# Kernel optimization log

Hardware: AMD Instinct MI355X
Metric: run time of the kernel (lower is better)

The kernel has to match this reference:

```python
import jax, jax.numpy as jnp
import numpy as np

GRAVITY, MAIN_THRUST, SIDE_TORQUE, DT = 10.0, 6.0, 1.0, 0.02
H_OBS = jnp.array([[1, 0, 0, 0, 0, 0],
                   [0, 1, 0, 0, 0, 0],
                   [0, 0, 0, 0, 1, 0]], dtype=jnp.float32)  # (3,6)


def build_psd(log_diag, off_diag, dim):
    rows, cols = np.tril_indices(dim, -1)  # row-major, same order as torch.tril_indices
    L = jnp.zeros((dim, dim), dtype=log_diag.dtype)
    L = L.at[jnp.arange(dim), jnp.arange(dim)].set(jnp.exp(log_diag))
    L = L.at[rows, cols].set(off_diag)
    return L @ L.T + 1e-6 * jnp.eye(dim, dtype=log_diag.dtype)


def setup_inputs() -> dict:
    key = jax.random.key(0)
    B = 524288
    ks = jax.random.split(key, 8)
    z = jax.random.normal(ks[0], (B, 3), dtype=jnp.float32)
    u = jax.random.uniform(ks[1], (B, 2), dtype=jnp.float32)
    x_prev = jax.random.normal(ks[2], (B, 6), dtype=jnp.float32)
    A = 0.1 * jax.random.normal(ks[3], (B, 6, 6), dtype=jnp.float32)
    P_prev = jnp.einsum('bij,bkj->bik', A, A) + 0.5 * jnp.eye(6, dtype=jnp.float32)
    q_log_diag = jnp.array([-3.0, -3.0, -2.0, -2.0, -3.0, -2.0], dtype=jnp.float32)
    q_off_diag = 0.01 * jax.random.normal(ks[4], (15,), dtype=jnp.float32)
    r_log_diag = jnp.array([-2.0, -2.0, -2.0], dtype=jnp.float32)
    r_off_diag = 0.01 * jax.random.normal(ks[5], (3,), dtype=jnp.float32)
    return {"z": z, "u": u, "x_prev": x_prev, "P_prev": P_prev,
            "q_log_diag": q_log_diag, "q_off_diag": q_off_diag,
            "r_log_diag": r_log_diag, "r_off_diag": r_off_diag}


def _dynamics(x, u):
    px, py, vx, vy, theta, omega = (x[:, i] for i in range(6))
    main_power = jnp.clip(u[:, 0], 0.0, 1.0)
    lateral = u[:, 1]
    sin_th, cos_th = jnp.sin(theta), jnp.cos(theta)
    ax = -MAIN_THRUST * sin_th * main_power
    ay = MAIN_THRUST * cos_th * main_power - GRAVITY
    alpha = SIDE_TORQUE * lateral
    new_vx = vx + ax * DT
    new_vy = vy + ay * DT
    new_omega = omega + alpha * DT
    new_px = px + new_vx * DT
    new_py = py + new_vy * DT
    new_theta = theta + new_omega * DT
    return jnp.stack([new_px, new_py, new_vx, new_vy, new_theta, new_omega], axis=-1)


def _dynamics_jacobian(x, u):
    B = x.shape[0]
    theta = x[:, 4]
    main_power = jnp.clip(u[:, 0], 0.0, 1.0)
    sin_th, cos_th = jnp.sin(theta), jnp.cos(theta)
    Tm = MAIN_THRUST * main_power
    d = jnp.arange(6)
    F = jnp.zeros((B, 6, 6), dtype=x.dtype).at[:, d, d].set(1.0)
    F = F.at[:, 0, 2].set(DT).at[:, 1, 3].set(DT).at[:, 4, 5].set(DT)
    F = F.at[:, 2, 4].set(-Tm * cos_th * DT)
    F = F.at[:, 3, 4].set(-Tm * sin_th * DT)
    F = F.at[:, 0, 4].set(-Tm * cos_th * (DT * DT))
    F = F.at[:, 1, 4].set(-Tm * sin_th * (DT * DT))
    return F


def reference(z, u, x_prev, P_prev, q_log_diag, q_off_diag, r_log_diag, r_off_diag):
    Q = build_psd(q_log_diag, q_off_diag, 6)
    R = build_psd(r_log_diag, r_off_diag, 3)
    H = H_OBS
    # predict
    x_pred = _dynamics(x_prev, u)                              # (B,6)
    F = _dynamics_jacobian(x_prev, u)                          # (B,6,6)
    P_pred = jnp.einsum('bij,bjk,blk->bil', F, P_prev, F) + Q  # F P F^T + Q
    # update
    z_pred = jnp.einsum('ij,bj->bi', H, x_pred)                # (B,3)
    y = z - z_pred
    HP = jnp.einsum('ij,bjk->bik', H, P_pred)                  # (B,3,6)
    S = jnp.einsum('bij,kj->bik', HP, H) + R                   # (B,3,3)
    K = jnp.swapaxes(jnp.linalg.solve(S, HP), -1, -2)          # (B,6,3)
    x_upd = x_pred + jnp.einsum('bij,bj->bi', K, y)
    IKH = jnp.eye(6, dtype=x_pred.dtype) - jnp.einsum('bij,jk->bik', K, H)
    P_upd = (jnp.einsum('bij,bjk,blk->bil', IKH, P_pred, IKH)
             + jnp.einsum('bij,jk,blk->bil', K, R, K))          # Joseph form
    return (x_upd, P_upd)
```

## Files before the change

### kernel.cpp

```cpp
#include <hip/hip_runtime.h>

namespace {
constexpr float GRAVITY     = 10.0f;
constexpr float MAIN_THRUST = 6.0f;
constexpr float DT          = 0.02f;
constexpr int   BLK         = 256;
constexpr int   CHUNK       = 256;
constexpr int   ROWPAD      = 44;
}

typedef float nfloat4 __attribute__((ext_vector_type(4)));
typedef float nfloat2 __attribute__((ext_vector_type(2)));

__global__ void qr_precompute(const float* __restrict__ qld,
                              const float* __restrict__ qod,
                              const float* __restrict__ rld,
                              const float* __restrict__ rod,
                              float* __restrict__ out)
{
    if (threadIdx.x != 0 || blockIdx.x != 0) return;
    float L[6][6];
    for (int i = 0; i < 6; ++i)
        for (int j = 0; j < 6; ++j) L[i][j] = 0.0f;
    for (int i = 0; i < 6; ++i) L[i][i] = expf(qld[i]);
    L[1][0] = qod[0];
    L[2][0] = qod[1];  L[2][1] = qod[2];
    L[3][0] = qod[3];  L[3][1] = qod[4];  L[3][2] = qod[5];
    L[4][0] = qod[6];  L[4][1] = qod[7];  L[4][2] = qod[8];  L[4][3] = qod[9];
    L[5][0] = qod[10]; L[5][1] = qod[11]; L[5][2] = qod[12]; L[5][3] = qod[13];
    L[5][4] = qod[14];
    for (int i = 0; i < 6; ++i)
        for (int j = 0; j < 6; ++j) {
            float s = 0.0f;
            const int m = i < j ? i : j;
            for (int k = 0; k <= m; ++k) s += L[i][k] * L[j][k];
            if (i == j) s += 1e-6f;
            out[i * 6 + j] = s;
        }
    const float rd0 = expf(rld[0]), rd1 = expf(rld[1]), rd2 = expf(rld[2]);
    const float ro0 = rod[0], ro1 = rod[1], ro2 = rod[2];
    out[36] = rd0 * rd0 + 1e-6f;
    out[37] = ro0 * rd0;
    out[38] = ro0 * ro0 + rd1 * rd1 + 1e-6f;
    out[39] = ro1 * rd0;
    out[40] = ro1 * ro0 + ro2 * rd1;
    out[41] = ro1 * ro1 + ro2 * ro2 + rd2 * rd2 + 1e-6f;
}

__device__ __forceinline__ void load_chunk(const nfloat4* __restrict__ gP4,
                                           int t, int count4, nfloat4 pf[9]) {
    #pragma unroll
    for (int k = 0; k < 9; ++k) {
        const int g4 = t + k * BLK;
        if (g4 < count4) pf[k] = __builtin_nontemporal_load(&gP4[g4]);
    }
}

__device__ __forceinline__ void stage_in(const nfloat4 pf[9], float* smem,
                                         int t, int count4) {
    #pragma unroll
    for (int k = 0; k < 9; ++k) {
        const int g4 = t + k * BLK;
        if (g4 < count4) {
            const int elem = g4 / 9;
            const int off4 = g4 % 9;
            *reinterpret_cast<nfloat4*>(&smem[elem * ROWPAD + off4 * 4]) = pf[k];
        }
    }
}

__device__ __forceinline__ void stage_out(nfloat4* __restrict__ oP4,
                                          const float* smem, int t, int count4) {
    #pragma unroll
    for (int k = 0; k < 9; ++k) {
        const int g4 = t + k * BLK;
        if (g4 < count4) {
            const int elem = g4 / 9;
            const int off4 = g4 % 9;
            const nfloat4 v = *reinterpret_cast<const nfloat4*>(&smem[elem * ROWPAD + off4 * 4]);
            __builtin_nontemporal_store(v, &oP4[g4]);
        }
    }
}

__global__ __launch_bounds__(BLK, 3) void ekf_kernel(
    const float* __restrict__ z,
    const float* __restrict__ u,
    const float* __restrict__ x_prev,
    const float* __restrict__ P_prev,
    const float* __restrict__ qr,
    float* __restrict__ x_out,
    float* __restrict__ P_out,
    int B)
{
    __shared__ float smem[BLK * ROWPAD];

    const int t  = threadIdx.x;
    const int c0 = blockIdx.x;
    const int c1 = blockIdx.x + gridDim.x;
    const int nchunk = (B + CHUNK - 1) / CHUNK;

    const int base0   = c0 * CHUNK;
    const int nE0     = min(B - base0, CHUNK);
    const int count40 = nE0 * 9;
    const bool has1   = (c1 < nchunk);
    const int base1   = has1 ? c1 * CHUNK : 0;
    const int nE1     = has1 ? min(B - base1, CHUNK) : 0;
    const int count41 = nE1 * 9;

    auto do_compute = [&](int base, int nE) {
        if (t >= nE) return;
        const int b = base + t;

        const float R00 = qr[36], R10 = qr[37], R11 = qr[38];
        const float R20 = qr[39], R21 = qr[40], R22 = qr[41];

        const nfloat2* xp2 = reinterpret_cast<const nfloat2*>(x_prev + 6 * b);
        const nfloat2 x01 = xp2[0], x23 = xp2[1], x45 = xp2[2];
        const float px = x01.x, py = x01.y, vx = x23.x, vy = x23.y;
        const float th = x45.x, om = x45.y;

        const nfloat2 uu = *reinterpret_cast<const nfloat2*>(u + 2 * b);
        const float mp  = fminf(fmaxf(uu.x, 0.0f), 1.0f);
        const float lat = uu.y;

        float s_th, c_th;
        __sincosf(th, &s_th, &c_th);

        const float Tm  = MAIN_THRUST * mp;
        const float ax  = -Tm * s_th;
        const float ay  =  Tm * c_th - GRAVITY;
        const float nvx = vx + ax * DT;
        const float nvy = vy + ay * DT;
        const float nom = om + lat * DT;
        const float npx = px + nvx * DT;
        const float npy = py + nvy * DT;
        const float nth = th + nom * DT;
        const float xp[6] = {npx, npy, nvx, nvy, nth, nom};

        const float f24 = -Tm * c_th * DT;
        const float f34 = -Tm * s_th * DT;
        const float f04 = f24 * DT;
        const float f14 = f34 * DT;

        float P[36];
        const float* myrow = &smem[t * ROWPAD];
        #pragma unroll
        for (int k = 0; k < 9; ++k) {
            const nfloat4 v = *reinterpret_cast<const nfloat4*>(&myrow[k * 4]);
            P[4 * k + 0] = v.x; P[4 * k + 1] = v.y;
            P[4 * k + 2] = v.z; P[4 * k + 3] = v.w;
        }

        #pragma unroll
        for (int j = 0; j < 6; ++j) {
            P[0 * 6 + j] += DT * P[2 * 6 + j] + f04 * P[4 * 6 + j];
            P[1 * 6 + j] += DT * P[3 * 6 + j] + f14 * P[4 * 6 + j];
            P[2 * 6 + j] += f24 * P[4 * 6 + j];
            P[3 * 6 + j] += f34 * P[4 * 6 + j];
            P[4 * 6 + j] += DT * P[5 * 6 + j];
        }
        #pragma unroll
        for (int i = 0; i < 6; ++i) {
            const float m0 = P[i * 6 + 0], m1 = P[i * 6 + 1], m2 = P[i * 6 + 2];
            const float m3 = P[i * 6 + 3], m4 = P[i * 6 + 4], m5 = P[i * 6 + 5];
            P[i * 6 + 0] = m0 + DT * m2 + f04 * m4 + qr[i * 6 + 0];
            P[i * 6 + 1] = m1 + DT * m3 + f14 * m4 + qr[i * 6 + 1];
            P[i * 6 + 2] = m2 + f24 * m4 + qr[i * 6 + 2];
            P[i * 6 + 3] = m3 + f34 * m4 + qr[i * 6 + 3];
            P[i * 6 + 4] = m4 + DT * m5 + qr[i * 6 + 4];
            P[i * 6 + 5] = m5 + qr[i * 6 + 5];
        }

        const float* zp = z + 3 * b;
        const float y0 = zp[0] - npx;
        const float y1 = zp[1] - npy;
        const float y2 = zp[2] - nth;

        const float s00 = P[0 * 6 + 0] + R00;
        const float s01 = P[0 * 6 + 1] + R10;
        const float s02 = P[0 * 6 + 4] + R20;
        const float s10 = P[1 * 6 + 0] + R10;
        const float s11 = P[1 * 6 + 1] + R11;
        const float s12 = P[1 * 6 + 4] + R21;
        const float s20 = P[4 * 6 + 0] + R20;
        const float s21 = P[4 * 6 + 1] + R21;
        const float s22 = P[4 * 6 + 4] + R22;

        const float det = s00 * (s11 * s22 - s12 * s21)
                        + s01 * (s12 * s20 - s10 * s22)
                        + s02 * (s10 * s21 - s11 * s20);
        const float invd = 1.0f / det;
        const float i00 = (s11 * s22 - s12 * s21) * invd;
        const float i01 = (s02 * s21 - s01 * s22) * invd;
        const float i02 = (s01 * s12 - s02 * s11) * invd;
        const float i10 = (s12 * s20 - s10 * s22) * invd;
        const float i11 = (s00 * s22 - s02 * s20) * invd;
        const float i12 = (s02 * s10 - s00 * s12) * invd;
        const float i20 = (s10 * s21 - s11 * s20) * invd;
        const float i21 = (s01 * s20 - s00 * s21) * invd;
        const float i22 = (s00 * s11 - s01 * s10) * invd;

        float r0[6], r1[6], r4[6];
        #pragma unroll
        for (int j = 0; j < 6; ++j) {
            r0[j] = P[0 * 6 + j];
            r1[j] = P[1 * 6 + j];
            r4[j] = P[4 * 6 + j];
        }

        float K[6][3];
        #pragma unroll
        for (int i = 0; i < 6; ++i) {
            const float hp0 = r0[i], hp1 = r1[i], hp2 = r4[i];
            K[i][0] = i00 * hp0 + i01 * hp1 + i02 * hp2;
            K[i][1] = i10 * hp0 + i11 * hp1 + i12 * hp2;
            K[i][2] = i20 * hp0 + i21 * hp1 + i22 * hp2;
        }

        nfloat2* xo2 = reinterpret_cast<nfloat2*>(x_out + 6 * b);
        float xu[6];
        #pragma unroll
        for (int i = 0; i < 6; ++i)
            xu[i] = xp[i] + K[i][0] * y0 + K[i][1] * y1 + K[i][2] * y2;
        nfloat2 o01; o01.x = xu[0]; o01.y = xu[1];
        nfloat2 o23; o23.x = xu[2]; o23.y = xu[3];
        nfloat2 o45; o45.x = xu[4]; o45.y = xu[5];
        __builtin_nontemporal_store(o01, &xo2[0]);
        __builtin_nontemporal_store(o23, &xo2[1]);
        __builtin_nontemporal_store(o45, &xo2[2]);

        #pragma unroll
        for (int i = 0; i < 6; ++i)
            #pragma unroll
            for (int j = 0; j < 6; ++j)
                P[i * 6 + j] -= K[i][0] * r0[j] + K[i][1] * r1[j] + K[i][2] * r4[j];

        float* myrowW = &smem[t * ROWPAD];
        #pragma unroll
        for (int k = 0; k < 9; ++k) {
            nfloat4 v;
            v.x = P[4 * k + 0]; v.y = P[4 * k + 1];
            v.z = P[4 * k + 2]; v.w = P[4 * k + 3];
            *reinterpret_cast<nfloat4*>(&myrowW[k * 4]) = v;
        }
    };

    nfloat4 pfA[9];
    load_chunk(reinterpret_cast<const nfloat4*>(P_prev + (size_t)base0 * 36),
               t, count40, pfA);

    stage_in(pfA, smem, t, count40);
    nfloat4 pfB[9];
    if (has1)
        load_chunk(reinterpret_cast<const nfloat4*>(P_prev + (size_t)base1 * 36),
                   t, count41, pfB);
    __syncthreads();
    do_compute(base0, nE0);
    __syncthreads();
    stage_out(reinterpret_cast<nfloat4*>(P_out + (size_t)base0 * 36),
              smem, t, count40);

    if (has1) {
        __syncthreads();
        stage_in(pfB, smem, t, count41);
        __syncthreads();
        do_compute(base1, nE1);
        __syncthreads();
        stage_out(reinterpret_cast<nfloat4*>(P_out + (size_t)base1 * 36),
                  smem, t, count41);
    }
}

extern "C" void kernel_launch(void* const* d_in, const int* in_sizes, int n_in,
                              void* d_out, int out_size, void* d_ws, size_t ws_size,
                              hipStream_t stream) {
    const float* z          = (const float*)d_in[0];
    const float* u          = (const float*)d_in[1];
    const float* x_prev     = (const float*)d_in[2];
    const float* P_prev     = (const float*)d_in[3];
    const float* q_log_diag = (const float*)d_in[4];
    const float* q_off_diag = (const float*)d_in[5];
    const float* r_log_diag = (const float*)d_in[6];
    const float* r_off_diag = (const float*)d_in[7];

    const int B = in_sizes[0] / 3;
    float* x_out = (float*)d_out;
    float* P_out = (float*)d_out + (size_t)B * 6;
    float* qrbuf = (float*)d_ws;

    qr_precompute<<<1, 64, 0, stream>>>(q_log_diag, q_off_diag,
                                        r_log_diag, r_off_diag, qrbuf);

    const int nchunk = (B + CHUNK - 1) / CHUNK;
    const int grid   = (nchunk + 1) / 2;
    ekf_kernel<<<grid, BLK, 0, stream>>>(z, u, x_prev, P_prev, qrbuf,
                                         x_out, P_out, B);
}
```

Measured before the change: 186.9 us.

## Use persistent grid-stride loop with register prefetch of next chunk

Replaces the fixed two-chunks-per-block scheme with a persistent kernel of at most 512 blocks that loops over chunks in grid-stride order. Each iteration prefetches the next chunk's covariance data into registers while computing the current one, so load latency overlaps with compute and the store phase. The nontemporal hint on P loads is also dropped in favour of plain loads. The risk is lower occupancy and parallelism: 512 blocks at 3 blocks per CU on a 256-CU device may not fill the GPU. The extra register set for the prefetch buffer also adds register pressure.

```diff
diff --git a/kernel.cpp b/kernel.cpp
--- a/kernel.cpp
+++ b/kernel.cpp
@@ -7,6 +7,7 @@
 constexpr int   BLK         = 256;
 constexpr int   CHUNK       = 256;
 constexpr int   ROWPAD      = 44;
+constexpr int   GRID        = 512;
 }
 
 typedef float nfloat4 __attribute__((ext_vector_type(4)));
@@ -52,7 +53,7 @@
     #pragma unroll
     for (int k = 0; k < 9; ++k) {
         const int g4 = t + k * BLK;
-        if (g4 < count4) pf[k] = __builtin_nontemporal_load(&gP4[g4]);
+        if (g4 < count4) pf[k] = gP4[g4];
     }
 }
 
@@ -95,18 +96,9 @@
 {
     __shared__ float smem[BLK * ROWPAD];
 
-    const int t  = threadIdx.x;
-    const int c0 = blockIdx.x;
-    const int c1 = blockIdx.x + gridDim.x;
+    const int t      = threadIdx.x;
     const int nchunk = (B + CHUNK - 1) / CHUNK;
-
-    const int base0   = c0 * CHUNK;
-    const int nE0     = min(B - base0, CHUNK);
-    const int count40 = nE0 * 9;
-    const bool has1   = (c1 < nchunk);
-    const int base1   = has1 ? c1 * CHUNK : 0;
-    const int nE1     = has1 ? min(B - base1, CHUNK) : 0;
-    const int count41 = nE1 * 9;
+    const int stride = gridDim.x;
 
     auto do_compute = [&](int base, int nE) {
         if (t >= nE) return;
@@ -246,29 +238,44 @@
         }
     };
 
+    int c = blockIdx.x;
+    if (c >= nchunk) return;
+
+    int base   = c * CHUNK;
+    int nE     = min(B - base, CHUNK);
+    int count4 = nE * 9;
+
     nfloat4 pfA[9];
-    load_chunk(reinterpret_cast<const nfloat4*>(P_prev + (size_t)base0 * 36),
-               t, count40, pfA);
-
-    stage_in(pfA, smem, t, count40);
-    nfloat4 pfB[9];
-    if (has1)
-        load_chunk(reinterpret_cast<const nfloat4*>(P_prev + (size_t)base1 * 36),
-                   t, count41, pfB);
-    __syncthreads();
-    do_compute(base0, nE0);
-    __syncthreads();
-    stage_out(reinterpret_cast<nfloat4*>(P_out + (size_t)base0 * 36),
-              smem, t, count40);
-
-    if (has1) {
+    load_chunk(reinterpret_cast<const nfloat4*>(P_prev + (size_t)base * 36),
+               t, count4, pfA);
+
+    for (;;) {
+        stage_in(pfA, smem, t, count4);
+
+        const int cn      = c + stride;
+        const bool hasN   = (cn < nchunk);
+        int baseN = 0, nEN = 0, count4N = 0;
+        nfloat4 pfB[9];
+        if (hasN) {
+            baseN   = cn * CHUNK;
+            nEN     = min(B - baseN, CHUNK);
+            count4N = nEN * 9;
+            load_chunk(reinterpret_cast<const nfloat4*>(P_prev + (size_t)baseN * 36),
+                       t, count4N, pfB);
+        }
+
         __syncthreads();
-        stage_in(pfB, smem, t, count41);
+        do_compute(base, nE);
         __syncthreads();
-        do_compute(base1, nE1);
+        stage_out(reinterpret_cast<nfloat4*>(P_out + (size_t)base * 36),
+                  smem, t, count4);
+
+        if (!hasN) break;
         __syncthreads();
-        stage_out(reinterpret_cast<nfloat4*>(P_out + (size_t)base1 * 36),
-                  smem, t, count41);
+
+        #pragma unroll
+        for (int k = 0; k < 9; ++k) pfA[k] = pfB[k];
+        c = cn; base = baseN; nE = nEN; count4 = count4N;
     }
 }
 
@@ -293,7 +300,7 @@
                                         r_log_diag, r_off_diag, qrbuf);
 
     const int nchunk = (B + CHUNK - 1) / CHUNK;
-    const int grid   = (nchunk + 1) / 2;
+    const int grid   = nchunk < GRID ? nchunk : GRID;
     ekf_kernel<<<grid, BLK, 0, stream>>>(z, u, x_prev, P_prev, qrbuf,
                                          x_out, P_out, B);
 }
```

After: 186.0 us. Within noise of the previous version (-0.4%).
